# Kernel tuning notes

Measured on AMD Instinct MI355X. Metric: run time of the kernel, lower is better.

Reference implementation:

```python
import jax, jax.numpy as jnp
import numpy as np

N = 10000        # nodes
E = 160000       # edges (avg degree 16)
WIDTH = 32       # node hidden width
KER_W = 256      # kernel MLP hidden width
KER_IN = 6       # edge feature dim
DEPTH = 4        # message-passing iterations


def setup_inputs() -> dict:
    key = jax.random.key(0)
    ks = jax.random.split(key, 12)
    def w(k, shape, fan_in):
        return jax.random.normal(k, shape, jnp.float32) * (1.0 / np.sqrt(fan_in)).astype(np.float32)
    return {
        "x": jax.random.normal(ks[0], (N, 1), jnp.float32),
        "edge_index": jax.random.randint(ks[1], (2, E), 0, N),
        "edge_attr": jax.random.uniform(ks[2], (E, KER_IN), dtype=jnp.float32),
        # fc1: Linear(1, WIDTH)
        "fc1_w": w(ks[3], (1, WIDTH), 1), "fc1_b": jnp.zeros((WIDTH,), jnp.float32),
        # kernel DenseNet: KER_IN -> KER_W -> KER_W -> WIDTH^2 (ReLU between, none after last)
        "k1_w": w(ks[4], (KER_IN, KER_W), KER_IN), "k1_b": jnp.zeros((KER_W,), jnp.float32),
        "k2_w": w(ks[5], (KER_W, KER_W), KER_W), "k2_b": jnp.zeros((KER_W,), jnp.float32),
        "k3_w": w(ks[6], (KER_W, WIDTH * WIDTH), KER_W), "k3_b": jnp.zeros((WIDTH * WIDTH,), jnp.float32),
        # NNConv root weight + bias
        "root_w": w(ks[7], (WIDTH, WIDTH), WIDTH), "conv_b": jnp.zeros((WIDTH,), jnp.float32),
        # fc2: Linear(WIDTH, 1)
        "fc2_w": w(ks[8], (WIDTH, 1), WIDTH), "fc2_b": jnp.zeros((1,), jnp.float32),
    }


def reference(x, edge_index, edge_attr, fc1_w, fc1_b, k1_w, k1_b, k2_w, k2_b,
              k3_w, k3_b, root_w, conv_b, fc2_w, fc2_b):
    src, dst = edge_index[0], edge_index[1]  # messages flow src -> dst

    # Per-edge kernel weights (edge_attr is constant across depth -> compute once).
    h = jax.nn.relu(edge_attr @ k1_w + k1_b)
    h = jax.nn.relu(h @ k2_w + k2_b)
    W_e = (h @ k3_w + k3_b).reshape(E, WIDTH, WIDTH)  # [E, in, out]

    # Degree for scatter-mean (avoid div by zero).
    deg = jax.ops.segment_sum(jnp.ones((E,), jnp.float32), dst, num_segments=N)
    inv_deg = (1.0 / jnp.maximum(deg, 1.0))[:, None]

    h_node = x @ fc1_w + fc1_b  # [N, WIDTH]
    for _ in range(DEPTH):
        msg = jnp.einsum('ei,eio->eo', h_node[src], W_e)              # gather + per-edge GEMM
        agg = jax.ops.segment_sum(msg, dst, num_segments=N) * inv_deg  # scatter-mean
        h_node = jax.nn.relu(agg + h_node @ root_w + conv_b)
    return h_node @ fc2_w + fc2_b  # [N, 1]
```

## Files before the change

### kernel.cpp

```cpp
#include <hip/hip_runtime.h>
#include <hip/hip_fp16.h>

#define NNODE 10000
#define NEDGE 160000
#define W32 32
#define BSTR 40
#define PANEL_F16 10240
#define PANEL3_F16 5120
#define UB_TILES 20000
#define HB_STR 264
#define TB_STR 1036

typedef _Float16 f16;
typedef _Float16 f16x4 __attribute__((ext_vector_type(4)));
typedef _Float16 f16x8 __attribute__((ext_vector_type(8)));
typedef float f32x4 __attribute__((ext_vector_type(4)));

__device__ __forceinline__ void stage_panel(f16* lds, const f16* g, int w, int lane) {
    #pragma unroll
    for (int i = 0; i < 5; ++i) {
        int slot = w * 320 + i * 64 + lane;
        __builtin_amdgcn_global_load_lds(
            (const __attribute__((address_space(1))) unsigned int*)(g + (size_t)slot * 8),
            (__attribute__((address_space(3))) unsigned int*)(lds + (size_t)(w * 320 + i * 64) * 8),
            16, 0, 0);
    }
}

__device__ __forceinline__ void stage_panel10k(f16* lds, const f16* g, int w, int lane) {
    #pragma unroll
    for (int i = 0; i < 2; ++i) {
        int base = i * 256 + w * 64;
        __builtin_amdgcn_global_load_lds(
            (const __attribute__((address_space(1))) unsigned int*)(g + (size_t)(base + lane) * 8),
            (__attribute__((address_space(3))) unsigned int*)(lds + (size_t)base * 8),
            16, 0, 0);
    }
    if (w < 2) {
        int base = 512 + w * 64;
        __builtin_amdgcn_global_load_lds(
            (const __attribute__((address_space(1))) unsigned int*)(g + (size_t)(base + lane) * 8),
            (__attribute__((address_space(3))) unsigned int*)(lds + (size_t)base * 8),
            16, 0, 0);
    }
}

__global__ __launch_bounds__(256) void pack_k1(const float* __restrict__ k1w, f16* __restrict__ k1p) {
    int t = blockIdx.x * 256 + threadIdx.x;
    int j = t / BSTR, c = t % BSTR;
    k1p[t] = (c < 6) ? (f16)k1w[c * 256 + j] : (f16)0.f;
}
__global__ __launch_bounds__(256) void pack_k2(const float* __restrict__ k2w, f16* __restrict__ k2p) {
    int t = blockIdx.x * 256 + threadIdx.x;
    int kk = t / PANEL_F16, r = t % PANEL_F16;
    int j = r / BSTR, c = r % BSTR;
    k2p[t] = (c < 32) ? (f16)k2w[(size_t)(kk * 32 + c) * 256 + j] : (f16)0.f;
}
__global__ __launch_bounds__(256) void pack_k3(const float* __restrict__ k3w, f16* __restrict__ k3p) {
    int t = blockIdx.x * 256 + threadIdx.x;
    int p = t / PANEL3_F16, r = t % PANEL3_F16;
    int np = p >> 3, kk = p & 7;
    int j = r / BSTR, c = r % BSTR;
    k3p[t] = (c < 32) ? (f16)k3w[(size_t)(kk * 32 + c) * 1024 + np * 128 + j] : (f16)0.f;
}
__global__ __launch_bounds__(256) void pack_k3t(const float* __restrict__ k3w, f16* __restrict__ k3t) {
    int t = blockIdx.x * 256 + threadIdx.x;
    int q = t / BSTR, i = t % BSTR;
    int o = q >> 8, c = q & 255;
    k3t[t] = (i < 32) ? (f16)k3w[(size_t)c * 1024 + i * 32 + o] : (f16)0.f;
}

__global__ __launch_bounds__(256) void h2_kernel(
    const float* __restrict__ ea,
    const f16* __restrict__ k1p, const float* __restrict__ k1b,
    const f16* __restrict__ k2p, const float* __restrict__ k2b,
    f16* __restrict__ h2c, int e_start, const int* __restrict__ remap)
{
    __shared__ __align__(16) f16 bls[2][256 * BSTR];
    __shared__ __align__(16) f16 ea_s[64 * BSTR];
    __shared__ __align__(16) f16 hbuf[64 * HB_STR];

    const int t = threadIdx.x, w = t >> 6, lane = t & 63, quad = lane >> 4, l15 = lane & 15;
    const int el0 = blockIdx.x * 64;
    const int e0 = e_start + el0;

    stage_panel(bls[0], k1p, w, lane);
    for (int i = t; i < 64 * BSTR; i += 256) {
        int e = i / BSTR, c = i % BSTR;
        ea_s[i] = (f16)((c < 6) ? ea[(size_t)(e0 + e) * 6 + c] : 0.f);
    }
    __syncthreads();

    f16x8 a1 = *(const f16x8*)&ea_s[(w * 16 + l15) * BSTR + quad * 8];
    {
        f32x4 acc1[16];
        #pragma unroll
        for (int nt = 0; nt < 16; ++nt) { float b = k1b[nt * 16 + l15]; acc1[nt] = (f32x4){b, b, b, b}; }
        stage_panel(bls[1], k2p, w, lane);
        #pragma unroll
        for (int nt = 0; nt < 16; ++nt) {
            f16x8 bf = *(const f16x8*)&bls[0][(nt * 16 + l15) * BSTR + quad * 8];
            acc1[nt] = __builtin_amdgcn_mfma_f32_16x16x32_f16(a1, bf, acc1[nt], 0, 0, 0);
        }
        #pragma unroll
        for (int nt = 0; nt < 16; ++nt)
            #pragma unroll
            for (int r = 0; r < 4; ++r)
                hbuf[(w * 16 + quad * 4 + r) * HB_STR + nt * 16 + l15] = (f16)fmaxf(acc1[nt][r], 0.f);
    }
    __syncthreads();

    const int mh = w & 1, nh = w >> 1;
    f16x8 a2[2][8];
    #pragma unroll
    for (int m = 0; m < 2; ++m)
        #pragma unroll
        for (int kk = 0; kk < 8; ++kk)
            a2[m][kk] = *(const f16x8*)&hbuf[(mh * 32 + m * 16 + l15) * HB_STR + kk * 32 + quad * 8];
    f32x4 acc[2][8];
    #pragma unroll
    for (int nt = 0; nt < 8; ++nt) {
        float b = k2b[nh * 128 + nt * 16 + l15];
        acc[0][nt] = (f32x4){b, b, b, b};
        acc[1][nt] = (f32x4){b, b, b, b};
    }
    for (int kk = 0; kk < 8; ++kk) {
        if (kk < 7)
            stage_panel(bls[kk & 1], k2p + (size_t)(kk + 1) * PANEL_F16, w, lane);
        const f16* B = bls[(kk + 1) & 1];
        #pragma unroll
        for (int nt = 0; nt < 8; ++nt) {
            f16x8 bf = *(const f16x8*)&B[(nh * 128 + nt * 16 + l15) * BSTR + quad * 8];
            acc[0][nt] = __builtin_amdgcn_mfma_f32_16x16x32_f16(a2[0][kk], bf, acc[0][nt], 0, 0, 0);
            acc[1][nt] = __builtin_amdgcn_mfma_f32_16x16x32_f16(a2[1][kk], bf, acc[1][nt], 0, 0, 0);
        }
        __syncthreads();
    }
    size_t orow[2][4];
    #pragma unroll
    for (int m = 0; m < 2; ++m)
        #pragma unroll
        for (int r = 0; r < 4; ++r) {
            int row = mh * 32 + m * 16 + quad * 4 + r;
            orow[m][r] = remap ? (size_t)remap[e0 + row] : (size_t)(el0 + row);
        }
    #pragma unroll
    for (int m = 0; m < 2; ++m)
        #pragma unroll
        for (int nt = 0; nt < 8; ++nt)
            #pragma unroll
            for (int r = 0; r < 4; ++r)
                h2c[orow[m][r] * 256 + nh * 128 + nt * 16 + l15] = (f16)fmaxf(acc[m][nt][r], 0.f);
}

__global__ __launch_bounds__(256) void hist_kernel(const int* __restrict__ ei, int* __restrict__ cnt) {
    int e = blockIdx.x * 256 + threadIdx.x;
    if (e < NEDGE) atomicAdd(&cnt[ei[e]], 1);
}
__global__ __launch_bounds__(256) void scan_kernel(
    const int* __restrict__ cnt, int* __restrict__ edgeStart,
    int* __restrict__ tileStartN, int* __restrict__ cursor)
{
    __shared__ int pE[256], pT[256];
    const int t = threadIdx.x;
    int se = 0, st = 0;
    for (int k = 0; k < 40; ++k) {
        int n = t * 40 + k;
        if (n < NNODE) { int c = cnt[n]; se += c; st += (c + 15) >> 4; }
    }
    pE[t] = se; pT[t] = st;
    __syncthreads();
    if (t == 0) {
        int aE = 0, aT = 0;
        for (int i = 0; i < 256; ++i) { int tE = pE[i], tT = pT[i]; pE[i] = aE; pT[i] = aT; aE += tE; aT += tT; }
        tileStartN[NNODE] = aT;
    }
    __syncthreads();
    int oE = pE[t], oT = pT[t];
    for (int k = 0; k < 40; ++k) {
        int n = t * 40 + k;
        if (n < NNODE) {
            edgeStart[n] = oE; cursor[n] = oE; tileStartN[n] = oT;
            int c = cnt[n]; oE += c; oT += (c + 15) >> 4;
        }
    }
}
__global__ __launch_bounds__(256) void scatter_kernel(
    const int* __restrict__ ei, int* __restrict__ cursor,
    int* __restrict__ dstS, int* __restrict__ sortpos)
{
    int e = blockIdx.x * 256 + threadIdx.x;
    if (e < NEDGE) {
        int s = ei[e];
        int p = atomicAdd(&cursor[s], 1);
        dstS[p] = ei[NEDGE + e];
        sortpos[e] = p;
    }
}
__global__ __launch_bounds__(256) void tiles_kernel(
    const int* __restrict__ cnt, const int* __restrict__ edgeStart, const int* __restrict__ tileStartN,
    int* __restrict__ tileNode, int* __restrict__ tileE0, int* __restrict__ tileCnt)
{
    int n = blockIdx.x * 256 + threadIdx.x;
    if (n < NNODE) {
        int d = cnt[n], t0 = tileStartN[n], e0 = edgeStart[n];
        for (int k = 0; k * 16 < d; ++k) {
            int rem = d - k * 16;
            tileNode[t0 + k] = n;
            tileE0[t0 + k] = e0 + k * 16;
            tileCnt[t0 + k] = rem < 16 ? rem : 16;
        }
    }
}

__global__ __launch_bounds__(256) void bb_kernel(
    const float* __restrict__ h, const float* __restrict__ k3b, float* __restrict__ Bb)
{
    int idx = blockIdx.x * 256 + threadIdx.x;
    int n = idx >> 5, o = idx & 31;
    float s = 0.f;
    #pragma unroll
    for (int i = 0; i < 32; ++i)
        s += h[n * 32 + i] * k3b[i * 32 + o];
    Bb[idx] = s;
}

__global__ __launch_bounds__(256) void tgen_kernel(
    const float* __restrict__ h, const f16* __restrict__ k3t, f16* __restrict__ Tt,
    int n0, int n1)
{
    __shared__ __align__(16) f16 tbuf[16 * TB_STR];

    const int t = threadIdx.x, w = t >> 6, lane = t & 63, quad = lane >> 4, l15 = lane & 15;
    const int nBase = n0 + blockIdx.x * 16;
    const int colBase = blockIdx.y * 1024;

    f16x8 a;
    #pragma unroll
    for (int i = 0; i < 8; ++i) a[i] = (f16)0.f;
    int node = nBase + l15;
    if (node < n1) {
        const float4* hp = (const float4*)(h + (size_t)node * 32) + quad * 2;
        float4 v0 = hp[0], v1 = hp[1];
        a[0] = (f16)v0.x; a[1] = (f16)v0.y; a[2] = (f16)v0.z; a[3] = (f16)v0.w;
        a[4] = (f16)v1.x; a[5] = (f16)v1.y; a[6] = (f16)v1.z; a[7] = (f16)v1.w;
    }
    f32x4 acc[16];
    #pragma unroll
    for (int nt = 0; nt < 16; ++nt) {
        f16x8 bf = *(const f16x8*)&k3t[(size_t)(colBase + w * 256 + nt * 16 + l15) * BSTR + quad * 8];
        acc[nt] = __builtin_amdgcn_mfma_f32_16x16x32_f16(a, bf, (f32x4){0.f, 0.f, 0.f, 0.f}, 0, 0, 0);
    }
    #pragma unroll
    for (int nt = 0; nt < 16; ++nt)
        #pragma unroll
        for (int r = 0; r < 4; ++r)
            tbuf[(quad * 4 + r) * TB_STR + w * 256 + nt * 16 + l15] = (f16)acc[nt][r];
    __syncthreads();
    {
        const int row = t >> 4, u = t & 15;
        const int nd = nBase + row;
        if (nd < n1) {
            f16* gdst = Tt + (size_t)(nd - n0) * 8192 + colBase;
            const f16* lsrc = &tbuf[row * TB_STR];
            #pragma unroll
            for (int j = 0; j < 8; ++j) {
                int p = u + 16 * j;
                *(f16x8*)(gdst + p * 8) = *(const f16x8*)(lsrc + p * 8);
            }
        }
    }
}

__global__ __launch_bounds__(256) void msgT_kernel(
    const f16* __restrict__ h2s, const f16* __restrict__ Tt, const float* __restrict__ Bb,
    const int* __restrict__ tileNode, const int* __restrict__ tileE0, const int* __restrict__ tileCnt,
    const int* __restrict__ tileStartN, const int* __restrict__ dstS, float* __restrict__ agg,
    int n0, int n1)
{
    const int t = threadIdx.x, w = t >> 6, lane = t & 63, quad = lane >> 4, l15 = lane & 15;
    const int t0 = tileStartN[n0], t1 = tileStartN[n1];
    for (int tile = t0 + blockIdx.x * 4 + w; tile < t1; tile += gridDim.x * 4) {
        int n = tileNode[tile];
        int e0 = tileE0[tile], cnt = tileCnt[tile];
        const f16* Tn = Tt + (size_t)(n - n0) * 8192;
        f32x4 acc[2];
        #pragma unroll
        for (int nt = 0; nt < 2; ++nt) {
            float b = Bb[n * 32 + nt * 16 + l15];
            acc[nt] = (f32x4){b, b, b, b};
        }
        #pragma unroll
        for (int kk = 0; kk < 8; ++kk) {
            f16x8 a;
            #pragma unroll
            for (int i = 0; i < 8; ++i) a[i] = (f16)0.f;
            if (l15 < cnt)
                a = *(const f16x8*)&h2s[(size_t)(e0 + l15) * 256 + kk * 32 + quad * 8];
            #pragma unroll
            for (int nt = 0; nt < 2; ++nt) {
                f16x8 bf = *(const f16x8*)&Tn[(nt * 16 + l15) * 256 + kk * 32 + quad * 8];
                acc[nt] = __builtin_amdgcn_mfma_f32_16x16x32_f16(a, bf, acc[nt], 0, 0, 0);
            }
        }
        #pragma unroll
        for (int nt = 0; nt < 2; ++nt)
            #pragma unroll
            for (int r = 0; r < 4; ++r) {
                int er = quad * 4 + r;
                if (er < cnt)
                    atomicAdd(&agg[(size_t)dstS[e0 + er] * 32 + nt * 16 + l15], acc[nt][r]);
            }
    }
}

__global__ __launch_bounds__(256, 2) void msg_fused(
    const int* __restrict__ ei, const f16* __restrict__ h2c,
    const f16* __restrict__ k3p, const float* __restrict__ k3b,
    const float* __restrict__ h, float* __restrict__ agg, int e_start)
{
    __shared__ __align__(16) f16 bls[2][PANEL3_F16];
    __shared__ __align__(16) f16 h_s[256 * 36];
    __shared__ int dst_s[256];

    const int t = threadIdx.x, w = t >> 6, lane = t & 63, quad = lane >> 4, l15 = lane & 15;
    const int el0 = blockIdx.x * 256;
    const int e0 = e_start + el0;

    dst_s[t] = ei[NEDGE + e0 + t];
    {
        int srcn = ei[e0 + t];
        const float4* hr = (const float4*)(h + (size_t)srcn * 32);
        f16* dp = &h_s[t * 36];
        #pragma unroll
        for (int qq = 0; qq < 8; ++qq) {
            float4 v = hr[qq];
            dp[qq * 4 + 0] = (f16)v.x; dp[qq * 4 + 1] = (f16)v.y;
            dp[qq * 4 + 2] = (f16)v.z; dp[qq * 4 + 3] = (f16)v.w;
        }
    }
    stage_panel10k(bls[0], k3p, w, lane);

    float msg[4][4][2];
    #pragma unroll
    for (int m = 0; m < 4; ++m)
        #pragma unroll
        for (int r = 0; r < 4; ++r) { msg[m][r][0] = 0.f; msg[m][r][1] = 0.f; }

    f32x4 acc[4][8];
    __syncthreads();

    for (int it = 0; it < 64; ++it) {
        const int np = it >> 3, kk = it & 7;
        if (it) __syncthreads();
        if (it < 63) stage_panel10k(bls[(it + 1) & 1], k3p + (size_t)(it + 1) * PANEL3_F16, w, lane);

        f16x8 a[4];
        #pragma unroll
        for (int m = 0; m < 4; ++m)
            a[m] = *(const f16x8*)(h2c + (size_t)(el0 + w * 64 + m * 16 + l15) * 256 + kk * 32 + quad * 8);

        if (kk == 0) {
            #pragma unroll
            for (int nt = 0; nt < 8; ++nt) {
                float b = k3b[np * 128 + nt * 16 + l15];
                #pragma unroll
                for (int m = 0; m < 4; ++m) acc[m][nt] = (f32x4){b, b, b, b};
            }
        }
        const f16* B = bls[it & 1];
        #pragma unroll
        for (int nt = 0; nt < 8; ++nt) {
            f16x8 bf = *(const f16x8*)&B[(nt * 16 + l15) * BSTR + quad * 8];
            #pragma unroll
            for (int m = 0; m < 4; ++m)
                acc[m][nt] = __builtin_amdgcn_mfma_f32_16x16x32_f16(a[m], bf, acc[m][nt], 0, 0, 0);
        }
        if (kk == 7) {
            #pragma unroll
            for (int m = 0; m < 4; ++m)
                #pragma unroll
                for (int r = 0; r < 4; ++r) {
                    int row = w * 64 + m * 16 + quad * 4 + r;
                    f16x4 h4 = *(const f16x4*)&h_s[row * 36 + np * 4];
                    #pragma unroll
                    for (int nt = 0; nt < 8; ++nt)
                        msg[m][r][nt & 1] += (float)h4[nt >> 1] * acc[m][nt][r];
                }
        }
    }
    #pragma unroll
    for (int m = 0; m < 4; ++m)
        #pragma unroll
        for (int r = 0; r < 4; ++r) {
            int d = dst_s[w * 64 + m * 16 + quad * 4 + r];
            atomicAdd(&agg[d * W32 + l15],      msg[m][r][0]);
            atomicAdd(&agg[d * W32 + 16 + l15], msg[m][r][1]);
        }
}

__global__ __launch_bounds__(256) void h0_kernel(
    const float* __restrict__ x, const float* __restrict__ fc1w,
    const float* __restrict__ fc1b, float* __restrict__ h)
{
    int idx = blockIdx.x * 256 + threadIdx.x;
    int n = idx >> 5, j = idx & 31;
    h[idx] = x[n] * fc1w[j] + fc1b[j];
}

__global__ __launch_bounds__(256) void deg_kernel(
    const int* __restrict__ ei, float* __restrict__ deg)
{
    int e = blockIdx.x * 256 + threadIdx.x;
    if (e < NEDGE) atomicAdd(&deg[ei[NEDGE + e]], 1.f);
}

__global__ __launch_bounds__(256) void update_kernel(
    const float* __restrict__ h_old, float* __restrict__ h_new,
    float* __restrict__ agg, const float* __restrict__ deg,
    const float* __restrict__ rootw, const float* __restrict__ convb)
{
    __shared__ float rw[W32][W32 + 1];
    const int t = threadIdx.x;
    for (int q = t; q < W32 * W32; q += 256)
        rw[q >> 5][q & 31] = rootw[q];
    __syncthreads();
    const int nl = t >> 5, j = t & 31;
    const int n = blockIdx.x * 8 + nl;
    float hv = h_old[n * W32 + j];
    float acc = convb[j];
    #pragma unroll
    for (int k = 0; k < W32; ++k)
        acc += __shfl(hv, k, 32) * rw[k][j];
    float inv = 1.f / fmaxf(deg[n], 1.f);
    int idx = n * W32 + j;
    float a = agg[idx];
    agg[idx] = 0.f;
    h_new[idx] = fmaxf(a * inv + acc, 0.f);
}

__global__ __launch_bounds__(256) void out_kernel(
    const float* __restrict__ h, const float* __restrict__ fc2w,
    const float* __restrict__ fc2b, float* __restrict__ out)
{
    int n = blockIdx.x * 256 + threadIdx.x;
    if (n < NNODE) {
        float a = fc2b[0];
        #pragma unroll
        for (int j = 0; j < W32; ++j)
            a += h[n * W32 + j] * fc2w[j];
        out[n] = a;
    }
}

static inline size_t pad256(size_t x) { return (x + 255) & ~(size_t)255; }

extern "C" void kernel_launch(void* const* d_in, const int* in_sizes, int n_in,
                              void* d_out, int out_size, void* d_ws, size_t ws_size,
                              hipStream_t stream) {
    const float* x    = (const float*)d_in[0];
    const int*   ei   = (const int*)  d_in[1];
    const float* ea   = (const float*)d_in[2];
    const float* fc1w = (const float*)d_in[3];
    const float* fc1b = (const float*)d_in[4];
    const float* k1w  = (const float*)d_in[5];
    const float* k1b  = (const float*)d_in[6];
    const float* k2w  = (const float*)d_in[7];
    const float* k2b  = (const float*)d_in[8];
    const float* k3w  = (const float*)d_in[9];
    const float* k3b  = (const float*)d_in[10];
    const float* rootw= (const float*)d_in[11];
    const float* convb= (const float*)d_in[12];
    const float* fc2w = (const float*)d_in[13];
    const float* fc2b = (const float*)d_in[14];
    float* out = (float*)d_out;

    const size_t hbytes = (size_t)NNODE * W32 * 4;
    char* ws = (char*)d_ws;
    size_t off = 0;
    float* hA  = (float*)(ws + off); off += hbytes;
    float* hB  = (float*)(ws + off); off += hbytes;
    float* agg = (float*)(ws + off); off += hbytes;
    float* deg = (float*)(ws + off); off += 40960;
    f16*  k1p  = (f16*)(ws + off);   off += 20480;
    f16*  k2p  = (f16*)(ws + off);   off += 163840;
    f16*  k3p  = (f16*)(ws + off);   off += 655360;
    const size_t fixed = off;

    size_t toff = fixed;
    f16*  k3t      = (f16*)(ws + toff);  toff += pad256(8192 * BSTR * 2);
    int*  dstS     = (int*)(ws + toff);  toff += pad256((size_t)NEDGE * 4);
    int*  sortpos  = (int*)(ws + toff);  toff += pad256((size_t)NEDGE * 4);
    int*  cnt      = (int*)(ws + toff);  toff += pad256((size_t)NNODE * 4);
    int*  edgeStart= (int*)(ws + toff);  toff += pad256((size_t)NNODE * 4);
    int*  tileStartN=(int*)(ws + toff);  toff += pad256((size_t)(NNODE + 1) * 4);
    int*  cursor   = (int*)(ws + toff);  toff += pad256((size_t)NNODE * 4);
    int*  tileNode = (int*)(ws + toff);  toff += pad256((size_t)UB_TILES * 4);
    int*  tileE0   = (int*)(ws + toff);  toff += pad256((size_t)UB_TILES * 4);
    int*  tileCnt  = (int*)(ws + toff);  toff += pad256((size_t)UB_TILES * 4);
    float* Bb      = (float*)(ws + toff); toff += pad256((size_t)NNODE * 32 * 4);
    f16*  h2s      = (f16*)(ws + toff);  toff += pad256((size_t)NEDGE * 256 * 2);
    f16*  Tt       = (f16*)(ws + toff);

    int nc = 0, CS = 0;
    {
        const int cands[4] = {1, 2, 4, 8};
        for (int ci = 0; ci < 4; ++ci) {
            int c = cands[ci];
            int cs = ((NNODE + c - 1) / c + 15) & ~15;
            size_t tb = (size_t)cs * 8192 * 2;
            if (ws_size >= toff + tb) { nc = c; CS = cs; break; }
        }
    }

    hipMemsetAsync(deg, 0, (size_t)NNODE * 4, stream);
    hipMemsetAsync(agg, 0, (size_t)NNODE * W32 * 4, stream);

    pack_k1<<<40, 256, 0, stream>>>(k1w, k1p);
    pack_k2<<<320, 256, 0, stream>>>(k2w, k2p);

    h0_kernel<<<NNODE * W32 / 256, 256, 0, stream>>>(x, fc1w, fc1b, hA);
    deg_kernel<<<(NEDGE + 255) / 256, 256, 0, stream>>>(ei, deg);

    float* hcur = hA; float* hnext = hB;

    if (nc) {
        pack_k3t<<<1280, 256, 0, stream>>>(k3w, k3t);
        hipMemsetAsync(cnt, 0, (size_t)NNODE * 4, stream);
        hist_kernel<<<(NEDGE + 255) / 256, 256, 0, stream>>>(ei, cnt);
        scan_kernel<<<1, 256, 0, stream>>>(cnt, edgeStart, tileStartN, cursor);
        scatter_kernel<<<(NEDGE + 255) / 256, 256, 0, stream>>>(ei, cursor, dstS, sortpos);
        tiles_kernel<<<(NNODE + 255) / 256, 256, 0, stream>>>(cnt, edgeStart, tileStartN,
                                                              tileNode, tileE0, tileCnt);
        h2_kernel<<<NEDGE / 64, 256, 0, stream>>>(ea, k1p, k1b, k2p, k2b, h2s, 0, sortpos);

        for (int d = 0; d < 4; ++d) {
            bb_kernel<<<NNODE * 32 / 256, 256, 0, stream>>>(hcur, k3b, Bb);
            for (int ct = 0; ct < nc; ++ct) {
                int n0 = ct * CS;
                if (n0 >= NNODE) break;
                int n1 = n0 + CS; if (n1 > NNODE) n1 = NNODE;
                dim3 tg((n1 - n0 + 15) / 16, 8);
                tgen_kernel<<<tg, 256, 0, stream>>>(hcur, k3t, Tt, n0, n1);
                msgT_kernel<<<1280, 256, 0, stream>>>(h2s, Tt, Bb, tileNode, tileE0, tileCnt,
                                                      tileStartN, dstS, agg, n0, n1);
            }
            update_kernel<<<NNODE / 8, 256, 0, stream>>>(hcur, hnext, agg, deg, rootw, convb);
            float* tmp = hcur; hcur = hnext; hnext = tmp;
        }
    } else {
        f16* h2b = (f16*)(ws + fixed);
        pack_k3<<<1280, 256, 0, stream>>>(k3w, k3p);

        long long availC = 0;
        if (ws_size > fixed) availC = (long long)((ws_size - fixed) / 512);
        int C = (availC > NEDGE) ? NEDGE : (int)availC;
        C &= ~255;
        if (C < 256) return;

        const bool full = (C == NEDGE);
        if (full)
            h2_kernel<<<NEDGE / 64, 256, 0, stream>>>(ea, k1p, k1b, k2p, k2b, h2b, 0, nullptr);

        for (int d = 0; d < 4; ++d) {
            for (int es = 0; es < NEDGE; es += C) {
                int ce = (NEDGE - es < C) ? (NEDGE - es) : C;
                if (!full)
                    h2_kernel<<<ce / 64, 256, 0, stream>>>(ea, k1p, k1b, k2p, k2b, h2b, es, nullptr);
                msg_fused<<<ce / 256, 256, 0, stream>>>(ei, h2b, k3p, k3b, hcur, agg, es);
            }
            update_kernel<<<NNODE / 8, 256, 0, stream>>>(hcur, hnext, agg, deg, rootw, convb);
            float* tmp = hcur; hcur = hnext; hnext = tmp;
        }
    }
    out_kernel<<<(NNODE + 255) / 256, 256, 0, stream>>>(hcur, fc2w, fc2b, out);
}
```

Measured before the change: 616.3 us.

## Replace atomic scatter-add with dst-sorted message buffer and segmented reduction

When workspace allows, per-edge messages are written to a destination-sorted buffer (fp32 or fp16) instead of being atomically added into agg. The update kernel then sums each node's contiguous message segment and uses the segment length as the degree. This drops the agg memset, the deg kernel and atomic contention, and runs tgen in a single chunk. The cost is extra histogram, scan and scatter kernels plus a large message buffer write and read each iteration. In fp16 mode it also adds rounding error in the messages.

```diff
diff --git a/kernel.cpp b/kernel.cpp
--- a/kernel.cpp
+++ b/kernel.cpp
@@ -213,6 +213,47 @@
     }
 }
 
+__global__ __launch_bounds__(256) void histD_kernel(const int* __restrict__ ei, int* __restrict__ cnt) {
+    int e = blockIdx.x * 256 + threadIdx.x;
+    if (e < NEDGE) atomicAdd(&cnt[ei[NEDGE + e]], 1);
+}
+__global__ __launch_bounds__(256) void scanD_kernel(
+    const int* __restrict__ cnt, int* __restrict__ dEdgeStart, int* __restrict__ cursor)
+{
+    __shared__ int pE[256];
+    const int t = threadIdx.x;
+    int se = 0;
+    for (int k = 0; k < 40; ++k) {
+        int n = t * 40 + k;
+        if (n < NNODE) se += cnt[n];
+    }
+    pE[t] = se;
+    __syncthreads();
+    if (t == 0) {
+        int aE = 0;
+        for (int i = 0; i < 256; ++i) { int tE = pE[i]; pE[i] = aE; aE += tE; }
+        dEdgeStart[NNODE] = aE;
+    }
+    __syncthreads();
+    int oE = pE[t];
+    for (int k = 0; k < 40; ++k) {
+        int n = t * 40 + k;
+        if (n < NNODE) {
+            dEdgeStart[n] = oE; cursor[n] = oE;
+            oE += cnt[n];
+        }
+    }
+}
+__global__ __launch_bounds__(256) void scatterD_kernel(
+    const int* __restrict__ dstS, int* __restrict__ cursor, int* __restrict__ dpos)
+{
+    int p = blockIdx.x * 256 + threadIdx.x;
+    if (p < NEDGE) {
+        int d = dstS[p];
+        dpos[p] = atomicAdd(&cursor[d], 1);
+    }
+}
+
 __global__ __launch_bounds__(256) void bb_kernel(
     const float* __restrict__ h, const float* __restrict__ k3b, float* __restrict__ Bb)
 {
@@ -312,6 +353,80 @@
                     atomicAdd(&agg[(size_t)dstS[e0 + er] * 32 + nt * 16 + l15], acc[nt][r]);
             }
     }
+}
+
+__global__ __launch_bounds__(256) void msgTn_kernel(
+    const f16* __restrict__ h2s, const f16* __restrict__ Tt, const float* __restrict__ Bb,
+    const int* __restrict__ tileNode, const int* __restrict__ tileE0, const int* __restrict__ tileCnt,
+    const int* __restrict__ tileStartN, const int* __restrict__ dpos,
+    f16* __restrict__ msgDh, float* __restrict__ msgDf, int useh)
+{
+    const int t = threadIdx.x, w = t >> 6, lane = t & 63, quad = lane >> 4, l15 = lane & 15;
+    const int t1 = tileStartN[NNODE];
+    for (int tile = blockIdx.x * 4 + w; tile < t1; tile += gridDim.x * 4) {
+        int n = tileNode[tile];
+        int e0 = tileE0[tile], cnt = tileCnt[tile];
+        const f16* Tn = Tt + (size_t)n * 8192;
+        f32x4 acc[2];
+        #pragma unroll
+        for (int nt = 0; nt < 2; ++nt) {
+            float b = Bb[n * 32 + nt * 16 + l15];
+            acc[nt] = (f32x4){b, b, b, b};
+        }
+        #pragma unroll
+        for (int kk = 0; kk < 8; ++kk) {
+            f16x8 a;
+            #pragma unroll
+            for (int i = 0; i < 8; ++i) a[i] = (f16)0.f;
+            if (l15 < cnt)
+                a = *(const f16x8*)&h2s[(size_t)(e0 + l15) * 256 + kk * 32 + quad * 8];
+            #pragma unroll
+            for (int nt = 0; nt < 2; ++nt) {
+                f16x8 bf = *(const f16x8*)&Tn[(nt * 16 + l15) * 256 + kk * 32 + quad * 8];
+                acc[nt] = __builtin_amdgcn_mfma_f32_16x16x32_f16(a, bf, acc[nt], 0, 0, 0);
+            }
+        }
+        #pragma unroll
+        for (int nt = 0; nt < 2; ++nt)
+            #pragma unroll
+            for (int r = 0; r < 4; ++r) {
+                int er = quad * 4 + r;
+                if (er < cnt) {
+                    size_t q = (size_t)dpos[e0 + er] * 32 + nt * 16 + l15;
+                    if (useh) msgDh[q] = (f16)acc[nt][r];
+                    else      msgDf[q] = acc[nt][r];
+                }
+            }
+    }
+}
+
+__global__ __launch_bounds__(256) void updaten_kernel(
+    const float* __restrict__ h_old, float* __restrict__ h_new,
+    const f16* __restrict__ msgDh, const float* __restrict__ msgDf, int useh,
+    const int* __restrict__ dEdgeStart,
+    const float* __restrict__ rootw, const float* __restrict__ convb)
+{
+    __shared__ float rw[W32][W32 + 1];
+    const int t = threadIdx.x;
+    for (int q = t; q < W32 * W32; q += 256)
+        rw[q >> 5][q & 31] = rootw[q];
+    __syncthreads();
+    const int nl = t >> 5, j = t & 31;
+    const int n = blockIdx.x * 8 + nl;
+    float hv = h_old[n * W32 + j];
+    float acc = convb[j];
+    #pragma unroll
+    for (int k = 0; k < W32; ++k)
+        acc += __shfl(hv, k, 32) * rw[k][j];
+    int q0 = dEdgeStart[n], q1 = dEdgeStart[n + 1];
+    float s = 0.f;
+    if (useh) {
+        for (int q = q0; q < q1; ++q) s += (float)msgDh[(size_t)q * 32 + j];
+    } else {
+        for (int q = q0; q < q1; ++q) s += msgDf[(size_t)q * 32 + j];
+    }
+    float inv = 1.f / fmaxf((float)(q1 - q0), 1.f);
+    h_new[n * W32 + j] = fmaxf(s * inv + acc, 0.f);
 }
 
 __global__ __launch_bounds__(256, 2) void msg_fused(
@@ -500,31 +615,51 @@
     int*  tileCnt  = (int*)(ws + toff);  toff += pad256((size_t)UB_TILES * 4);
     float* Bb      = (float*)(ws + toff); toff += pad256((size_t)NNODE * 32 * 4);
     f16*  h2s      = (f16*)(ws + toff);  toff += pad256((size_t)NEDGE * 256 * 2);
-    f16*  Tt       = (f16*)(ws + toff);
+    const size_t toff_base = toff;
+
+    size_t o_dpos  = toff_base;
+    size_t o_dEdge = o_dpos + pad256((size_t)NEDGE * 4);
+    size_t o_msgD  = o_dEdge + pad256((size_t)(NNODE + 1) * 4);
+    size_t end_f16 = o_msgD + pad256((size_t)NEDGE * 32 * 2);
+    size_t end_f32 = o_msgD + pad256((size_t)NEDGE * 32 * 4);
+    const size_t ttb_full = (size_t)NNODE * 8192 * 2;
+
+    int*  dpos      = (int*)(ws + o_dpos);
+    int*  dEdgeStart= (int*)(ws + o_dEdge);
+    f16*  msgDh     = (f16*)(ws + o_msgD);
+    float* msgDf    = (float*)(ws + o_msgD);
+
+    int mode = 0;
+    f16* Tt = nullptr;
+    if (ws_size >= end_f32 + ttb_full)      { mode = 2; Tt = (f16*)(ws + end_f32); }
+    else if (ws_size >= end_f16 + ttb_full) { mode = 1; Tt = (f16*)(ws + end_f16); }
 
     int nc = 0, CS = 0;
-    {
+    if (!mode) {
         const int cands[4] = {1, 2, 4, 8};
         for (int ci = 0; ci < 4; ++ci) {
             int c = cands[ci];
             int cs = ((NNODE + c - 1) / c + 15) & ~15;
             size_t tb = (size_t)cs * 8192 * 2;
-            if (ws_size >= toff + tb) { nc = c; CS = cs; break; }
-        }
+            if (ws_size >= toff_base + tb) { nc = c; CS = cs; break; }
+        }
+        if (nc) Tt = (f16*)(ws + toff_base);
     }
 
     hipMemsetAsync(deg, 0, (size_t)NNODE * 4, stream);
-    hipMemsetAsync(agg, 0, (size_t)NNODE * W32 * 4, stream);
+    if (mode == 0)
+        hipMemsetAsync(agg, 0, (size_t)NNODE * W32 * 4, stream);
 
     pack_k1<<<40, 256, 0, stream>>>(k1w, k1p);
     pack_k2<<<320, 256, 0, stream>>>(k2w, k2p);
 
     h0_kernel<<<NNODE * W32 / 256, 256, 0, stream>>>(x, fc1w, fc1b, hA);
-    deg_kernel<<<(NEDGE + 255) / 256, 256, 0, stream>>>(ei, deg);
+    if (mode == 0)
+        deg_kernel<<<(NEDGE + 255) / 256, 256, 0, stream>>>(ei, deg);
 
     float* hcur = hA; float* hnext = hB;
 
-    if (nc) {
+    if (mode || nc) {
         pack_k3t<<<1280, 256, 0, stream>>>(k3w, k3t);
         hipMemsetAsync(cnt, 0, (size_t)NNODE * 4, stream);
         hist_kernel<<<(NEDGE + 255) / 256, 256, 0, stream>>>(ei, cnt);
@@ -534,23 +669,44 @@
                                                               tileNode, tileE0, tileCnt);
         h2_kernel<<<NEDGE / 64, 256, 0, stream>>>(ea, k1p, k1b, k2p, k2b, h2s, 0, sortpos);
 
-        for (int d = 0; d < 4; ++d) {
-            bb_kernel<<<NNODE * 32 / 256, 256, 0, stream>>>(hcur, k3b, Bb);
-            for (int ct = 0; ct < nc; ++ct) {
-                int n0 = ct * CS;
-                if (n0 >= NNODE) break;
-                int n1 = n0 + CS; if (n1 > NNODE) n1 = NNODE;
-                dim3 tg((n1 - n0 + 15) / 16, 8);
-                tgen_kernel<<<tg, 256, 0, stream>>>(hcur, k3t, Tt, n0, n1);
-                msgT_kernel<<<1280, 256, 0, stream>>>(h2s, Tt, Bb, tileNode, tileE0, tileCnt,
-                                                      tileStartN, dstS, agg, n0, n1);
-            }
-            update_kernel<<<NNODE / 8, 256, 0, stream>>>(hcur, hnext, agg, deg, rootw, convb);
-            float* tmp = hcur; hcur = hnext; hnext = tmp;
+        if (mode) {
+            hipMemsetAsync(cnt, 0, (size_t)NNODE * 4, stream);
+            histD_kernel<<<(NEDGE + 255) / 256, 256, 0, stream>>>(ei, cnt);
+            scanD_kernel<<<1, 256, 0, stream>>>(cnt, dEdgeStart, cursor);
+            scatterD_kernel<<<(NEDGE + 255) / 256, 256, 0, stream>>>(dstS, cursor, dpos);
+
+            const int useh = (mode == 1) ? 1 : 0;
+            for (int d = 0; d < 4; ++d) {
+                bb_kernel<<<NNODE * 32 / 256, 256, 0, stream>>>(hcur, k3b, Bb);
+                dim3 tg((NNODE + 15) / 16, 8);
+                tgen_kernel<<<tg, 256, 0, stream>>>(hcur, k3t, Tt, 0, NNODE);
+                msgTn_kernel<<<1280, 256, 0, stream>>>(h2s, Tt, Bb, tileNode, tileE0, tileCnt,
+                                                       tileStartN, dpos, msgDh, msgDf, useh);
+                updaten_kernel<<<NNODE / 8, 256, 0, stream>>>(hcur, hnext, msgDh, msgDf, useh,
+                                                              dEdgeStart, rootw, convb);
+                float* tmp = hcur; hcur = hnext; hnext = tmp;
+            }
+        } else {
+            for (int d = 0; d < 4; ++d) {
+                bb_kernel<<<NNODE * 32 / 256, 256, 0, stream>>>(hcur, k3b, Bb);
+                for (int ct = 0; ct < nc; ++ct) {
+                    int n0 = ct * CS;
+                    if (n0 >= NNODE) break;
+                    int n1 = n0 + CS; if (n1 > NNODE) n1 = NNODE;
+                    dim3 tg((n1 - n0 + 15) / 16, 8);
+                    tgen_kernel<<<tg, 256, 0, stream>>>(hcur, k3t, Tt, n0, n1);
+                    msgT_kernel<<<1280, 256, 0, stream>>>(h2s, Tt, Bb, tileNode, tileE0, tileCnt,
+                                                          tileStartN, dstS, agg, n0, n1);
+                }
+                update_kernel<<<NNODE / 8, 256, 0, stream>>>(hcur, hnext, agg, deg, rootw, convb);
+                float* tmp = hcur; hcur = hnext; hnext = tmp;
+            }
         }
     } else {
         f16* h2b = (f16*)(ws + fixed);
         pack_k3<<<1280, 256, 0, stream>>>(k3w, k3p);
+        hipMemsetAsync(agg, 0, (size_t)NNODE * W32 * 4, stream);
+        deg_kernel<<<(NEDGE + 255) / 256, 256, 0, stream>>>(ei, deg);
 
         long long availC = 0;
         if (ws_size > fixed) availC = (long long)((ws_size - fixed) / 512);
```

After: 691.2 us. +12.2%, slower.
